# Kernel tuning notes

Hardware: AMD Instinct MI355X
Metric: run time of the kernel (lower is better)

The kernel has to match this reference:

```python
import jax, jax.numpy as jnp
import numpy as np
from jax import lax

BITWIDTH = 7
EPS = 1e-5


def ti_quant(x):
    """TiFloatToInt8: per-tensor int8 quantization with power-of-2 scale."""
    rng = jnp.max(jnp.abs(x))
    bw = jnp.ceil(jnp.log2(rng))
    exp = bw - BITWIDTH
    q = jnp.clip(jnp.round(x * 2.0 ** (BITWIDTH - bw)), -128.0, 127.0)
    return q, exp


def ti_conv(xv, xe, wv, we, pad):
    """TiConv2d: integer conv (simulated in f32, all values int-valued),
    int32 accumulate, then shift back to 8 bits; exponents add."""
    acc = lax.conv_general_dilated(
        xv, wv, window_strides=(1, 1), padding=[(pad, pad), (pad, pad)],
        dimension_numbers=("NCHW", "OIHW", "NCHW"))
    rng = jnp.max(jnp.abs(acc))
    bw = jnp.ceil(jnp.log2(rng))
    shift = jnp.maximum(bw - BITWIDTH, 0.0)
    q = jnp.clip(jnp.round(acc * 2.0 ** (-shift)), -128.0, 127.0)
    return q, xe + we + shift


def batchnorm(x, gamma, beta):
    # training-mode BN: batch statistics over (N, H, W)
    mean = jnp.mean(x, axis=(0, 2, 3), keepdims=True)
    var = jnp.var(x, axis=(0, 2, 3), keepdims=True)
    g = gamma[None, :, None, None]
    b = beta[None, :, None, None]
    return g * (x - mean) * lax.rsqrt(var + EPS) + b


def setup_inputs() -> dict:
    key = jax.random.key(0)
    k0, k1, k2, k3, k4 = jax.random.split(key, 5)
    B, Cin, Cout, H, W = 32, 128, 256, 56, 56
    x_val = jax.random.randint(k0, (B, Cin, H, W), -128, 128, dtype=jnp.int32)
    x_exp = jnp.zeros((), jnp.float32) - 7.0
    wDW = jnp.round(jnp.clip(jax.random.normal(k1, (Cin, Cin, 3, 3), jnp.float32) * 32.0, -128.0, 127.0))
    wDW_exp = jnp.zeros((), jnp.float32) - 9.0
    wPW = jnp.round(jnp.clip(jax.random.normal(k2, (Cout, Cin, 1, 1), jnp.float32) * 32.0, -128.0, 127.0))
    wPW_exp = jnp.zeros((), jnp.float32) - 9.0
    gamma1 = jnp.ones((Cin,), jnp.float32) + 0.1 * jax.random.normal(k3, (Cin,), jnp.float32)
    beta1 = jnp.zeros((Cin,), jnp.float32)
    gamma2 = jnp.ones((Cout,), jnp.float32) + 0.1 * jax.random.normal(k4, (Cout,), jnp.float32)
    beta2 = jnp.zeros((Cout,), jnp.float32)
    return {"x_val": x_val, "x_exp": x_exp, "wDW": wDW, "wDW_exp": wDW_exp,
            "wPW": wPW, "wPW_exp": wPW_exp, "gamma1": gamma1, "beta1": beta1,
            "gamma2": gamma2, "beta2": beta2}


def reference(x_val, x_exp, wDW, wDW_exp, wPW, wPW_exp, gamma1, beta1, gamma2, beta2):
    xv = x_val.astype(jnp.float32)
    # convDW (3x3, in->in, pad=1)
    q, e = ti_conv(xv, x_exp, wDW, wDW_exp, 1)
    # dequant -> bn1 -> quant
    f = batchnorm(q * 2.0 ** e, gamma1, beta1)
    q, e = ti_quant(f)
    # TiReLU on int values
    q = jnp.maximum(q, 0.0)
    # convPW (1x1, in->out)
    q, e = ti_conv(q, e, wPW, wPW_exp, 0)
    # dequant -> bn2 -> quant -> relu
    f = batchnorm(q * 2.0 ** e, gamma2, beta2)
    q, e = ti_quant(f)
    q = jnp.maximum(q, 0.0)
    return q.astype(jnp.int8), e
```

## Files before the change

### kernel.cpp

```cpp
#include <hip/hip_runtime.h>
#include <cstdint>
#include <cstddef>

#define C1 128
#define C2 256
#define Hh 56
#define Wd 56
#define HW 3136
#define NHW 100352
#define N1 ((size_t)12845056)
#define N2 ((size_t)25690112)
#define XPSZ ((size_t)13778944)
#define NREP 8

typedef int v4i __attribute__((ext_vector_type(4)));
typedef int v16i __attribute__((ext_vector_type(16)));

static constexpr size_t OFF_XP = 0;
static constexpr size_t OFF_ACC1 = XPSZ;
static constexpr size_t OFF_Q1 = OFF_ACC1 + 4 * N1;
static constexpr size_t OFF_Q3 = OFF_Q1 + N1;
static constexpr size_t OFF_WQ1 = OFF_Q3 + N2;
static constexpr size_t OFF_WQ2 = OFF_WQ1 + 147456;
static constexpr size_t OFF_STATS = OFF_WQ2 + 32768;

struct Stats {
  int absmax1, absmax2, tick1, tick2;
  float scale1, e1, s2, e2;
  float scaleq2, e3, sf, ef;
  int sum1[NREP][C1]; unsigned sumsq1[NREP][C1];
  int min1[NREP][C1], max1[NREP][C1];
  float A1[C1], B1c[C1];
  int sum2[NREP][C2]; unsigned sumsq2[NREP][C2];
  int min2[NREP][C2], max2[NREP][C2];
  float A2[C2], B2c[C2];
};

__global__ __launch_bounds__(256) void k_pre(
    const int* __restrict__ x, signed char* __restrict__ xp,
    const float* __restrict__ wDW, signed char* __restrict__ wq1t,
    const float* __restrict__ wPW, signed char* __restrict__ wq2t,
    Stats* st) {
  __shared__ signed char lds[56 * 132];
  int t = threadIdx.x, bid = blockIdx.x;
  if (bid < 1856) {
    int hh = bid % 58, n = bid / 58;
    int* xpw = (int*)(xp + ((size_t)n * 58 + hh) * 7424);
    if (hh == 0 || hh == 57) {
      for (int o = t; o < 1856; o += 256) xpw[o] = 0;
      return;
    }
    int h = hh - 1;
    const int* xb = x + (size_t)n * C1 * HW + h * 56;
    for (int idx = t; idx < 7168; idx += 256) {
      int c = idx / 56, w = idx - c * 56;
      lds[w * 132 + c] = (signed char)xb[(size_t)c * HW + w];
    }
    __syncthreads();
    for (int o = t; o < 1856; o += 256) {
      int kb = o / 232, r = o - kb * 232, ww = r >> 2, cw = r & 3;
      int val = (ww == 0 || ww == 57) ? 0
                : *(const int*)&lds[(ww - 1) * 132 + kb * 16 + cw * 4];
      xpw[o] = val;
    }
    return;
  }
  if (bid < 2432) {
    int idx = (bid - 1856) * 256 + t;
    int co = idx / 1152, r = idx - co * 1152;
    int ci = r / 9, pos = r - ci * 9;
    int k = pos * 128 + ci;
    wq1t[(size_t)(k >> 4) * 2048 + co * 16 + (k & 15)] = (signed char)(int)wDW[idx];
    return;
  }
  if (bid < 2560) {
    int i = (bid - 2432) * 256 + t;
    int co = i >> 7, ci = i & 127;
    wq2t[(size_t)(ci >> 4) * 4096 + co * 16 + (ci & 15)] = (signed char)(int)wPW[i];
    return;
  }
  if (t == 0) { st->absmax1 = 0; st->absmax2 = 0; st->tick1 = 0; st->tick2 = 0; }
  for (int c = t; c < NREP * C1; c += 256) {
    ((int*)st->sum1)[c] = 0; ((unsigned*)st->sumsq1)[c] = 0u;
    ((int*)st->min1)[c] = 127; ((int*)st->max1)[c] = -128;
  }
  for (int c = t; c < NREP * C2; c += 256) {
    ((int*)st->sum2)[c] = 0; ((unsigned*)st->sumsq2)[c] = 0u;
    ((int*)st->min2)[c] = 127; ((int*)st->max2)[c] = -128;
  }
}

__device__ inline v4i ld16_lds(const signed char* p) {
  const int2* q = (const int2*)p;
  int2 lo = q[0], hi = q[1];
  v4i r; r[0] = lo.x; r[1] = lo.y; r[2] = hi.x; r[3] = hi.y;
  return r;
}

__device__ inline float bn_affine_v(int sum, unsigned sumsq, int mn, int mx,
                                    float g, float b, float e_in,
                                    float* Aout, float* Bout) {
  double meanq = (double)sum / (double)NHW;
  double varq = (double)sumsq / (double)NHW - meanq * meanq;
  float se = exp2f(e_in);
  float mean = (float)meanq * se;
  float var = (float)varq * se * se;
  float rsq = 1.0f / sqrtf(var + 1e-5f);
  float Avv = g * se * rsq;
  float Bvv = b - g * mean * rsq;
  *Aout = Avv; *Bout = Bvv;
  return fmaxf(fabsf(Avv * (float)mn + Bvv), fabsf(Avv * (float)mx + Bvv));
}

__global__ __launch_bounds__(256, 2) void k_conv1s(
    const signed char* __restrict__ xp, const signed char* __restrict__ wq1t,
    int* __restrict__ acc1, Stats* st) {
  __shared__ int reda[4];
  int t = threadIdx.x, lane = t & 63, wave = t >> 6;
  int half = lane >> 5, l31 = lane & 31;
  size_t g0 = (size_t)blockIdx.x * 256;

  const signed char* ab[2];
#pragma unroll
  for (int i = 0; i < 2; ++i) {
    size_t gm = g0 + wave * 64 + i * 32 + l31;
    int n = (int)(gm / HW);
    int p = (int)(gm - (size_t)n * HW);
    int h = p / 56, w = p - h * 56;
    ab[i] = xp + ((size_t)n * 58 + h) * 7424 + w * 16 + half * 928;
  }
  const signed char* bb[4];
#pragma unroll
  for (int j = 0; j < 4; ++j)
    bb[j] = wq1t + (size_t)(j * 32 + l31) * 16 + half * 2048;

  v16i a1[2][4];
#pragma unroll
  for (int i = 0; i < 2; ++i)
#pragma unroll
    for (int j = 0; j < 4; ++j)
#pragma unroll
      for (int r = 0; r < 16; ++r) a1[i][j][r] = 0;

#pragma unroll
  for (int pos = 0; pos < 9; ++pos) {
    int kh = pos / 3, kw = pos - kh * 3;
    const signed char* a0p = ab[0] + kh * 7424 + kw * 16;
    const signed char* a1p = ab[1] + kh * 7424 + kw * 16;
#pragma unroll
    for (int kb = 0; kb < 8; kb += 2) {
      v4i af0 = *(const v4i*)(a0p + kb * 928);
      v4i af1 = *(const v4i*)(a1p + kb * 928);
      v4i bf[4];
#pragma unroll
      for (int j = 0; j < 4; ++j)
        bf[j] = *(const v4i*)(bb[j] + pos * 16384 + kb * 2048);
#pragma unroll
      for (int j = 0; j < 4; ++j) {
        a1[0][j] = __builtin_amdgcn_mfma_i32_32x32x32_i8(af0, bf[j], a1[0][j], 0, 0, 0);
        a1[1][j] = __builtin_amdgcn_mfma_i32_32x32x32_i8(af1, bf[j], a1[1][j], 0, 0, 0);
      }
    }
  }

  int am = 0;
#pragma unroll
  for (int i = 0; i < 2; ++i)
#pragma unroll
    for (int j = 0; j < 4; ++j)
#pragma unroll
      for (int r = 0; r < 16; ++r) am = max(am, abs(a1[i][j][r]));
  for (int off = 32; off; off >>= 1) am = max(am, __shfl_down(am, off, 64));
  if (lane == 0) reda[wave] = am;
  __syncthreads();
  if (t == 0)
    atomicMax(&st->absmax1, max(max(reda[0], reda[1]), max(reda[2], reda[3])));

  int* ob = acc1 + (size_t)blockIdx.x * 32768;
#pragma unroll
  for (int i = 0; i < 2; ++i)
#pragma unroll
    for (int j = 0; j < 4; ++j)
#pragma unroll
      for (int reg = 0; reg < 16; ++reg)
        ob[(((wave * 2 + i) * 4 + j) * 16 + reg) * 64 + lane] = a1[i][j][reg];
}

__global__ __launch_bounds__(256, 2) void k_qstats1(
    const int* __restrict__ acc1, signed char* __restrict__ q1, Stats* st,
    const float* __restrict__ x_exp, const float* __restrict__ wDW_exp,
    const float* __restrict__ gamma1, const float* __restrict__ beta1) {
  __shared__ int qti[256 * 34];
  __shared__ int psum[C1], psq[C1], pmn[C1], pmx[C1];
  __shared__ float redc[2];
  __shared__ int lastf;
  signed char* qt = (signed char*)qti;
  int t = threadIdx.x, lane = t & 63, wave = t >> 6;
  int half = lane >> 5, l31 = lane & 31;
  int rep = blockIdx.x & (NREP - 1);

  if (t < C1) { psum[t] = 0; psq[t] = 0; pmn[t] = 127; pmx[t] = -128; }
  __syncthreads();

  int v1 = st->absmax1;
  int pw = 31 - __clz(v1 | 1);
  int bw = ((v1 & (v1 - 1)) == 0) ? pw : pw + 1;
  int sh = max(bw - 7, 0);
  float scale1 = exp2f((float)(-sh));
  float e1 = x_exp[0] + wDW_exp[0] + (float)sh;
  if (blockIdx.x == 0 && t == 0) st->e1 = e1;

  const int* ib = acc1 + (size_t)blockIdx.x * 32768;
#pragma unroll
  for (int j = 0; j < 4; ++j) {
    int sj = 0, sqj = 0, mnj = 127, mxj = -128;
    int c = j * 32 + l31;
#pragma unroll
    for (int i = 0; i < 2; ++i)
#pragma unroll
      for (int reg = 0; reg < 16; ++reg) {
        int av = ib[(((wave * 2 + i) * 4 + j) * 16 + reg) * 64 + lane];
        int row = (reg & 3) + 8 * (reg >> 2) + 4 * half;
        int pix = wave * 64 + i * 32 + row;
        float r = rintf((float)av * scale1);
        r = fminf(fmaxf(r, -128.f), 127.f);
        int qi = (int)r;
        qt[pix * 136 + c] = (signed char)qi;
        sj += qi; sqj += qi * qi; mnj = min(mnj, qi); mxj = max(mxj, qi);
      }
    sj += __shfl_down(sj, 32, 64);
    sqj += __shfl_down(sqj, 32, 64);
    mnj = min(mnj, __shfl_down(mnj, 32, 64));
    mxj = max(mxj, __shfl_down(mxj, 32, 64));
    if (half == 0) {
      atomicAdd(&psum[c], sj); atomicAdd(&psq[c], sqj);
      atomicMin(&pmn[c], mnj); atomicMax(&pmx[c], mxj);
    }
  }
  __syncthreads();
  if (t < C1) {
    atomicAdd(&st->sum1[rep][t], psum[t]);
    atomicAdd(&st->sumsq1[rep][t], (unsigned)psq[t]);
    atomicMin(&st->min1[rep][t], pmn[t]);
    atomicMax(&st->max1[rep][t], pmx[t]);
  }
  int* q1w = (int*)(q1 + (size_t)blockIdx.x * 256 * 128);
  for (int idx = t; idx < 8192; idx += 256)
    q1w[idx] = qti[(idx >> 5) * 34 + (idx & 31)];

  __syncthreads();
  if (t == 0) lastf = (atomicAdd(&st->tick1, 1) == 391);
  __syncthreads();
  if (lastf) {
    if (t < C1) {
      int sm = 0; unsigned sq = 0; int mn = 127, mx = -128;
#pragma unroll
      for (int r2 = 0; r2 < NREP; ++r2) {
        sm += atomicAdd(&st->sum1[r2][t], 0);
        sq += atomicAdd(&st->sumsq1[r2][t], 0u);
        mn = min(mn, atomicMin(&st->min1[r2][t], 127));
        mx = max(mx, atomicMax(&st->max1[r2][t], -128));
      }
      float cand = bn_affine_v(sm, sq, mn, mx, gamma1[t], beta1[t], e1,
                               &st->A1[t], &st->B1c[t]);
      for (int off = 32; off; off >>= 1) cand = fmaxf(cand, __shfl_down(cand, off, 64));
      if ((t & 63) == 0) redc[t >> 6] = cand;
    }
    __syncthreads();
    if (t == 0) {
      float rng = fmaxf(redc[0], redc[1]);
      float bwv = ceilf(log2f(rng));
      st->s2 = exp2f(7.0f - bwv);
      st->e2 = bwv - 7.0f;
    }
  }
}

template <int STORE>
__global__ __launch_bounds__(256, 2) void k_conv2t(
    const signed char* __restrict__ q1, const signed char* __restrict__ wq2t,
    signed char* __restrict__ q3, Stats* st, const float* __restrict__ wPW_exp,
    const float* __restrict__ gamma2, const float* __restrict__ beta2,
    float* __restrict__ out) {
  __shared__ int qti[128 * 34];
  __shared__ signed char stg[128 * 264];
  __shared__ int psum[C2], psq[C2], pmn[C2], pmx[C2];
  __shared__ int reda[4];
  __shared__ float red2[4];
  __shared__ int lastf;
  signed char* qt = (signed char*)qti;

  int t = threadIdx.x, lane = t & 63, wave = t >> 6;
  int half = lane >> 5, l31 = lane & 31;
  size_t g0 = (size_t)blockIdx.x * 128;
  int rep = blockIdx.x & (NREP - 1);

  if (STORE) { psum[t] = 0; psq[t] = 0; pmn[t] = 127; pmx[t] = -128; }

  int c4 = t & 31;
  float Av[4], Bv[4];
#pragma unroll
  for (int jj = 0; jj < 4; ++jj) {
    Av[jj] = st->A1[c4 * 4 + jj];
    Bv[jj] = st->B1c[c4 * 4 + jj];
  }
  float s2 = st->s2;
  const int* q1w = (const int*)(q1 + g0 * 128);
#pragma unroll
  for (int k = 0; k < 16; ++k) {
    int idx = k * 256 + t;
    int v = q1w[idx];
    int pix = idx >> 5;
    int outv = 0;
#pragma unroll
    for (int jj = 0; jj < 4; ++jj) {
      int b = (signed char)(v >> (8 * jj));
      float y = Av[jj] * (float)b + Bv[jj];
      float r = rintf(y * s2);
      r = fminf(fmaxf(r, -128.f), 127.f);
      r = fmaxf(r, 0.f);
      outv |= ((int)r & 0xff) << (8 * jj);
    }
    qti[pix * 34 + c4] = outv;
  }
  __syncthreads();

  v16i acc[8];
#pragma unroll
  for (int j = 0; j < 8; ++j)
#pragma unroll
    for (int r = 0; r < 16; ++r) acc[j][r] = 0;

#pragma unroll
  for (int ks = 0; ks < 4; ++ks) {
    v4i af = ld16_lds(&qt[(wave * 32 + l31) * 136 + half * 16 + ks * 32]);
#pragma unroll
    for (int j = 0; j < 8; ++j) {
      v4i bf = *(const v4i*)(wq2t + (size_t)(ks * 2 + half) * 4096 + (j * 32 + l31) * 16);
      acc[j] = __builtin_amdgcn_mfma_i32_32x32x32_i8(af, bf, acc[j], 0, 0, 0);
    }
  }

  if (STORE == 0) {
    int am2 = 0;
#pragma unroll
    for (int j = 0; j < 8; ++j)
#pragma unroll
      for (int r = 0; r < 16; ++r) am2 = max(am2, abs(acc[j][r]));
    for (int off = 32; off; off >>= 1) am2 = max(am2, __shfl_down(am2, off, 64));
    if (lane == 0) reda[wave] = am2;
    __syncthreads();
    if (t == 0)
      atomicMax(&st->absmax2, max(max(reda[0], reda[1]), max(reda[2], reda[3])));
  } else {
    int v2 = st->absmax2;
    int pw = 31 - __clz(v2 | 1);
    int bw = ((v2 & (v2 - 1)) == 0) ? pw : pw + 1;
    int sh2 = max(bw - 7, 0);
    float scale2 = exp2f((float)(-sh2));
    float e3 = st->e2 + wPW_exp[0] + (float)sh2;
    if (blockIdx.x == 0 && t == 0) st->e3 = e3;
#pragma unroll
    for (int j = 0; j < 8; ++j) {
      int c = j * 32 + l31;
      int sj = 0, sqj = 0, mnj = 127, mxj = -128;
#pragma unroll
      for (int reg = 0; reg < 16; ++reg) {
        int row = (reg & 3) + 8 * (reg >> 2) + 4 * half;
        float r = rintf((float)acc[j][reg] * scale2);
        r = fminf(fmaxf(r, -128.f), 127.f);
        int qi = (int)r;
        stg[(wave * 32 + row) * 264 + c] = (signed char)qi;
        sj += qi; sqj += qi * qi; mnj = min(mnj, qi); mxj = max(mxj, qi);
      }
      sj += __shfl_down(sj, 32, 64);
      sqj += __shfl_down(sqj, 32, 64);
      mnj = min(mnj, __shfl_down(mnj, 32, 64));
      mxj = max(mxj, __shfl_down(mxj, 32, 64));
      if (half == 0) {
        atomicAdd(&psum[c], sj); atomicAdd(&psq[c], sqj);
        atomicMin(&pmn[c], mnj); atomicMax(&pmx[c], mxj);
      }
    }
    __syncthreads();
    atomicAdd(&st->sum2[rep][t], psum[t]);
    atomicAdd(&st->sumsq2[rep][t], (unsigned)psq[t]);
    atomicMin(&st->min2[rep][t], pmn[t]);
    atomicMax(&st->max2[rep][t], pmx[t]);
    int* q3w = (int*)(q3 + g0 * 256);
#pragma unroll
    for (int k = 0; k < 32; ++k) {
      int idx = k * 256 + t;
      int pix = idx >> 6, cw = idx & 63;
      q3w[idx] = *(const int*)&stg[pix * 264 + cw * 4];
    }

    __syncthreads();
    if (t == 0) lastf = (atomicAdd(&st->tick2, 1) == 783);
    __syncthreads();
    if (lastf) {
      int sm = 0; unsigned sq = 0; int mn = 127, mx = -128;
#pragma unroll
      for (int r2 = 0; r2 < NREP; ++r2) {
        sm += atomicAdd(&st->sum2[r2][t], 0);
        sq += atomicAdd(&st->sumsq2[r2][t], 0u);
        mn = min(mn, atomicMin(&st->min2[r2][t], 127));
        mx = max(mx, atomicMax(&st->max2[r2][t], -128));
      }
      float cand = bn_affine_v(sm, sq, mn, mx, gamma2[t], beta2[t], e3,
                               &st->A2[t], &st->B2c[t]);
      for (int off = 32; off; off >>= 1) cand = fmaxf(cand, __shfl_down(cand, off, 64));
      if (lane == 0) red2[wave] = cand;
      __syncthreads();
      if (t == 0) {
        float rng = fmaxf(fmaxf(red2[0], red2[1]), fmaxf(red2[2], red2[3]));
        float bwv = ceilf(log2f(rng));
        st->sf = exp2f(7.0f - bwv);
        st->ef = bwv - 7.0f;
        out[N2] = bwv - 7.0f;
      }
    }
  }
}

__global__ __launch_bounds__(256) void k_out(
    const signed char* __restrict__ q3, const Stats* __restrict__ st,
    float* __restrict__ out) {
  __shared__ signed char lds[64 * 260];
  int t = threadIdx.x, lane = t & 63, wave = t >> 6;
  size_t g0 = (size_t)blockIdx.x * 64;
  int n = (int)(g0 / HW), p0 = (int)(g0 - (size_t)n * HW);
  const int* q3w = (const int*)(q3 + g0 * 256);
#pragma unroll
  for (int k = 0; k < 16; ++k) {
    int idx = k * 256 + t;
    int pix = idx >> 6, cw = idx & 63;
    *(int*)&lds[pix * 260 + cw * 4] = q3w[idx];
  }
  __syncthreads();
  float sf = st->sf;
  float* ob = out + (size_t)n * C2 * HW + p0 + lane;
#pragma unroll
  for (int cg = 0; cg < 16; ++cg) {
    int v = *(const int*)&lds[lane * 260 + wave * 64 + cg * 4];
#pragma unroll
    for (int jj = 0; jj < 4; ++jj) {
      int c = wave * 64 + cg * 4 + jj;
      float y = st->A2[c] * (float)((signed char)(v >> (8 * jj))) + st->B2c[c];
      float r = rintf(y * sf);
      r = fminf(fmaxf(r, -128.f), 127.f);
      ob[(size_t)c * HW] = fmaxf(r, 0.f);
    }
  }
}

extern "C" void kernel_launch(void* const* d_in, const int* in_sizes, int n_in,
                              void* d_out, int out_size, void* d_ws, size_t ws_size,
                              hipStream_t stream) {
  const int* x = (const int*)d_in[0];
  const float* x_exp = (const float*)d_in[1];
  const float* wDW = (const float*)d_in[2];
  const float* wDW_exp = (const float*)d_in[3];
  const float* wPW = (const float*)d_in[4];
  const float* wPW_exp = (const float*)d_in[5];
  const float* gamma1 = (const float*)d_in[6];
  const float* beta1 = (const float*)d_in[7];
  const float* gamma2 = (const float*)d_in[8];
  const float* beta2 = (const float*)d_in[9];
  float* out = (float*)d_out;

  char* ws = (char*)d_ws;
  signed char* xp2 = (signed char*)(ws + OFF_XP);
  int* acc1 = (int*)(ws + OFF_ACC1);
  signed char* q1 = (signed char*)(ws + OFF_Q1);
  signed char* q3 = (signed char*)(ws + OFF_Q3);
  signed char* wq1t = (signed char*)(ws + OFF_WQ1);
  signed char* wq2t = (signed char*)(ws + OFF_WQ2);
  Stats* st = (Stats*)(ws + OFF_STATS);

  hipLaunchKernelGGL(k_pre, dim3(2561), dim3(256), 0, stream,
                     x, xp2, wDW, wq1t, wPW, wq2t, st);
  hipLaunchKernelGGL(k_conv1s, dim3(392), dim3(256), 0, stream,
                     xp2, wq1t, acc1, st);
  hipLaunchKernelGGL(k_qstats1, dim3(392), dim3(256), 0, stream,
                     acc1, q1, st, x_exp, wDW_exp, gamma1, beta1);
  hipLaunchKernelGGL(HIP_KERNEL_NAME(k_conv2t<0>), dim3(784), dim3(256), 0, stream,
                     q1, wq2t, q3, st, wPW_exp, gamma2, beta2, out);
  hipLaunchKernelGGL(HIP_KERNEL_NAME(k_conv2t<1>), dim3(784), dim3(256), 0, stream,
                     q1, wq2t, q3, st, wPW_exp, gamma2, beta2, out);
  hipLaunchKernelGGL(k_out, dim3(1568), dim3(256), 0, stream, q3, st, out);
}
```

Baseline: 276.9 us.

## Stage PW weights in LDS and store conv2 output in MFMA-native layout

The 1x1 conv kernel now copies the transposed PW weights into shared memory once per block and prefetches q1 into registers, so the MFMA inner loop reads B fragments from LDS instead of global memory. The intermediate q3 buffer is written directly in the MFMA accumulator register layout as packed int words, which removes the LDS staging transpose and a barrier-bound copy loop. The output kernel is rewritten to decode this layout through a padded LDS tile before emitting NCHW floats. The cost is more LDS per block for the 32KB weight copy, which may lower occupancy, plus a more complex index mapping in k_out.

```diff
diff --git a/kernel.cpp b/kernel.cpp
--- a/kernel.cpp
+++ b/kernel.cpp
@@ -282,8 +282,8 @@
     signed char* __restrict__ q3, Stats* st, const float* __restrict__ wPW_exp,
     const float* __restrict__ gamma2, const float* __restrict__ beta2,
     float* __restrict__ out) {
+  __shared__ __align__(16) signed char wq2s[32768];
   __shared__ int qti[128 * 34];
-  __shared__ signed char stg[128 * 264];
   __shared__ int psum[C2], psq[C2], pmn[C2], pmx[C2];
   __shared__ int reda[4];
   __shared__ float red2[4];
@@ -295,6 +295,15 @@
   size_t g0 = (size_t)blockIdx.x * 128;
   int rep = blockIdx.x & (NREP - 1);
 
+  v4i wtmp[8];
+#pragma unroll
+  for (int i = 0; i < 8; ++i)
+    wtmp[i] = *(const v4i*)(wq2t + i * 4096 + t * 16);
+  const int* q1w = (const int*)(q1 + g0 * 128);
+  int qv[16];
+#pragma unroll
+  for (int k = 0; k < 16; ++k) qv[k] = q1w[k * 256 + t];
+
   if (STORE) { psum[t] = 0; psq[t] = 0; pmn[t] = 127; pmx[t] = -128; }
 
   int c4 = t & 31;
@@ -305,12 +314,15 @@
     Bv[jj] = st->B1c[c4 * 4 + jj];
   }
   float s2 = st->s2;
-  const int* q1w = (const int*)(q1 + g0 * 128);
+
+#pragma unroll
+  for (int i = 0; i < 8; ++i)
+    *(v4i*)(wq2s + i * 4096 + t * 16) = wtmp[i];
+
 #pragma unroll
   for (int k = 0; k < 16; ++k) {
-    int idx = k * 256 + t;
-    int v = q1w[idx];
-    int pix = idx >> 5;
+    int v = qv[k];
+    int pix = (k * 256 + t) >> 5;
     int outv = 0;
 #pragma unroll
     for (int jj = 0; jj < 4; ++jj) {
@@ -336,7 +348,7 @@
     v4i af = ld16_lds(&qt[(wave * 32 + l31) * 136 + half * 16 + ks * 32]);
 #pragma unroll
     for (int j = 0; j < 8; ++j) {
-      v4i bf = *(const v4i*)(wq2t + (size_t)(ks * 2 + half) * 4096 + (j * 32 + l31) * 16);
+      v4i bf = *(const v4i*)(wq2s + (size_t)(ks * 2 + half) * 4096 + (j * 32 + l31) * 16);
       acc[j] = __builtin_amdgcn_mfma_i32_32x32x32_i8(af, bf, acc[j], 0, 0, 0);
     }
   }
@@ -360,18 +372,23 @@
     float scale2 = exp2f((float)(-sh2));
     float e3 = st->e2 + wPW_exp[0] + (float)sh2;
     if (blockIdx.x == 0 && t == 0) st->e3 = e3;
+    int* q3w = (int*)(q3 + (size_t)blockIdx.x * 32768);
 #pragma unroll
     for (int j = 0; j < 8; ++j) {
       int c = j * 32 + l31;
       int sj = 0, sqj = 0, mnj = 127, mxj = -128;
 #pragma unroll
-      for (int reg = 0; reg < 16; ++reg) {
-        int row = (reg & 3) + 8 * (reg >> 2) + 4 * half;
-        float r = rintf((float)acc[j][reg] * scale2);
-        r = fminf(fmaxf(r, -128.f), 127.f);
-        int qi = (int)r;
-        stg[(wave * 32 + row) * 264 + c] = (signed char)qi;
-        sj += qi; sqj += qi * qi; mnj = min(mnj, qi); mxj = max(mxj, qi);
+      for (int rg = 0; rg < 4; ++rg) {
+        int pk = 0;
+#pragma unroll
+        for (int b = 0; b < 4; ++b) {
+          float r = rintf((float)acc[j][4 * rg + b] * scale2);
+          r = fminf(fmaxf(r, -128.f), 127.f);
+          int qi = (int)r;
+          pk |= (qi & 0xff) << (8 * b);
+          sj += qi; sqj += qi * qi; mnj = min(mnj, qi); mxj = max(mxj, qi);
+        }
+        q3w[((wave * 8 + j) * 4 + rg) * 64 + lane] = pk;
       }
       sj += __shfl_down(sj, 32, 64);
       sqj += __shfl_down(sqj, 32, 64);
@@ -387,13 +404,6 @@
     atomicAdd(&st->sumsq2[rep][t], (unsigned)psq[t]);
     atomicMin(&st->min2[rep][t], pmn[t]);
     atomicMax(&st->max2[rep][t], pmx[t]);
-    int* q3w = (int*)(q3 + g0 * 256);
-#pragma unroll
-    for (int k = 0; k < 32; ++k) {
-      int idx = k * 256 + t;
-      int pix = idx >> 6, cw = idx & 63;
-      q3w[idx] = *(const int*)&stg[pix * 264 + cw * 4];
-    }
 
     __syncthreads();
     if (t == 0) lastf = (atomicAdd(&st->tick2, 1) == 783);
@@ -426,31 +436,32 @@
 __global__ __launch_bounds__(256) void k_out(
     const signed char* __restrict__ q3, const Stats* __restrict__ st,
     float* __restrict__ out) {
-  __shared__ signed char lds[64 * 260];
+  __shared__ int ldsc[256 * 17];
   int t = threadIdx.x, lane = t & 63, wave = t >> 6;
-  size_t g0 = (size_t)blockIdx.x * 64;
+  int bid = blockIdx.x;
+  size_t g0 = (size_t)bid * 64;
   int n = (int)(g0 / HW), p0 = (int)(g0 - (size_t)n * HW);
-  const int* q3w = (const int*)(q3 + g0 * 256);
+  const int* q3r = (const int*)(q3 + (size_t)(bid >> 1) * 32768) + (bid & 1) * 4096;
 #pragma unroll
   for (int k = 0; k < 16; ++k) {
-    int idx = k * 256 + t;
-    int pix = idx >> 6, cw = idx & 63;
-    *(int*)&lds[pix * 260 + cw * 4] = q3w[idx];
+    int i = k * 256 + t;
+    int ln = i & 63, rg = (i >> 6) & 3, j = (i >> 8) & 7, wv = (i >> 11) & 1;
+    int v = q3r[i];
+    int c = j * 32 + (ln & 31);
+    int psub = wv * 8 + 2 * rg + (ln >> 5);
+    ldsc[c * 17 + psub] = v;
   }
   __syncthreads();
   float sf = st->sf;
   float* ob = out + (size_t)n * C2 * HW + p0 + lane;
 #pragma unroll
-  for (int cg = 0; cg < 16; ++cg) {
-    int v = *(const int*)&lds[lane * 260 + wave * 64 + cg * 4];
-#pragma unroll
-    for (int jj = 0; jj < 4; ++jj) {
-      int c = wave * 64 + cg * 4 + jj;
-      float y = st->A2[c] * (float)((signed char)(v >> (8 * jj))) + st->B2c[c];
-      float r = rintf(y * sf);
-      r = fminf(fmaxf(r, -128.f), 127.f);
-      ob[(size_t)c * HW] = fmaxf(r, 0.f);
-    }
+  for (int cg = 0; cg < 64; ++cg) {
+    int c = wave * 64 + ((cg + wave * 16) & 63);
+    int vv = ldsc[c * 17 + (lane >> 2)];
+    float y = st->A2[c] * (float)((signed char)(vv >> (8 * (lane & 3)))) + st->B2c[c];
+    float r = rintf(y * sf);
+    r = fminf(fmaxf(r, -128.f), 127.f);
+    ob[(size_t)c * HW] = fmaxf(r, 0.f);
   }
 }
 
```

Measured after the change: 271.4 us. 2.0% less time.
